# Kernel optimization log

Measured on AMD Instinct MI355X. Metric: run time of the kernel, lower is better.

Reference implementation:

```python
import jax, jax.numpy as jnp
import numpy as np

NUM_HEADS = 12


def setup_inputs() -> dict:
    key = jax.random.key(0)
    ks = jax.random.split(key, 5)
    B, S, D = 4, 2048, 768
    scale = 0.02
    return {
        "hidden_states": jax.random.normal(ks[0], (B, S, D), dtype=jnp.float32),
        "c_attn_w": jax.random.normal(ks[1], (D, 3 * D), dtype=jnp.float32) * scale,
        "c_attn_b": jax.random.normal(ks[2], (3 * D,), dtype=jnp.float32) * scale,
        "c_proj_w": jax.random.normal(ks[3], (D, D), dtype=jnp.float32) * scale,
        "c_proj_b": jax.random.normal(ks[4], (D,), dtype=jnp.float32) * scale,
    }


def reference(hidden_states, c_attn_w, c_attn_b, c_proj_w, c_proj_b):
    B, S, D = hidden_states.shape
    H = NUM_HEADS
    hd = D // H

    # fused QKV projection (HF Conv1D: x @ W + b, W is [in, out])
    qkv = hidden_states @ c_attn_w + c_attn_b  # [B, S, 3D]
    q, k, v = jnp.split(qkv, 3, axis=-1)

    def split_heads(t):
        return t.reshape(B, S, H, hd).transpose(0, 2, 1, 3)  # [B, H, S, hd]

    q, k, v = split_heads(q), split_heads(k), split_heads(v)

    # scaled dot-product scores (scale_attn_weights=True -> / sqrt(head_dim))
    scores = jnp.einsum("bhqd,bhkd->bhqk", q, k) / jnp.asarray(
        np.sqrt(hd), dtype=q.dtype
    )

    # causal mask: where(tril, scores, dtype_min) as in eager GPT2Attention
    causal = jnp.tril(jnp.ones((S, S), dtype=bool))
    mask_value = jnp.finfo(scores.dtype).min
    scores = jnp.where(causal[None, None, :, :], scores, mask_value)

    attn = jax.nn.softmax(scores, axis=-1)  # attn_dropout p=0 (eval)

    out = jnp.einsum("bhqk,bhkd->bhqd", attn, v)
    out = out.transpose(0, 2, 1, 3).reshape(B, S, D)  # merge heads

    # output projection (resid_dropout p=0)
    return out @ c_proj_w + c_proj_b
```

## Files before the change

### kernel.cpp

```cpp
#include <hip/hip_runtime.h>
#include <stdint.h>

typedef __attribute__((ext_vector_type(8))) short short8;
typedef __attribute__((ext_vector_type(4))) short short4v;
typedef __attribute__((ext_vector_type(8))) __bf16 bf16x8;
typedef __attribute__((ext_vector_type(4))) float f32x4;

#define SEQ 2048
#define DMODEL 768
#define NHEAD 12
#define HD 64
#define NBATCH 4

#define QSCALE 0.18033688011112042f

__device__ __forceinline__ float bf2f(unsigned short u) {
    return __uint_as_float(((unsigned int)u) << 16);
}
__device__ __forceinline__ unsigned short f2bf(float f) {
    unsigned int u = __float_as_uint(f);
    u += 0x7fffu + ((u >> 16) & 1u);
    return (unsigned short)(u >> 16);
}
__device__ __forceinline__ unsigned short f2bfn(float f) {
    union { __bf16 h; unsigned short u; } cv;
    cv.h = (__bf16)f;
    return cv.u;
}
__device__ __forceinline__ short8 cvt8(float4 a, float4 b) {
    short8 r;
    r[0] = (short)f2bf(a.x); r[1] = (short)f2bf(a.y);
    r[2] = (short)f2bf(a.z); r[3] = (short)f2bf(a.w);
    r[4] = (short)f2bf(b.x); r[5] = (short)f2bf(b.y);
    r[6] = (short)f2bf(b.z); r[7] = (short)f2bf(b.w);
    return r;
}
__device__ __forceinline__ f32x4 mfma16(short8 a, short8 b, f32x4 c) {
    return __builtin_amdgcn_mfma_f32_16x16x32_bf16(
        __builtin_bit_cast(bf16x8, a), __builtin_bit_cast(bf16x8, b), c, 0, 0, 0);
}
__device__ __forceinline__ f32x4 mfma16k16(short4v a, short4v b, f32x4 c) {
#if __has_builtin(__builtin_amdgcn_mfma_f32_16x16x16bf16_1k)
    return __builtin_amdgcn_mfma_f32_16x16x16bf16_1k(a, b, c, 0, 0, 0);
#else
    asm("v_mfma_f32_16x16x16_bf16 %0, %1, %2, %0" : "+v"(c) : "v"(a), "v"(b));
    return c;
#endif
}
__device__ __forceinline__ void gload16(const unsigned short* g, unsigned short* l) {
    __builtin_amdgcn_global_load_lds(
        (const __attribute__((address_space(1))) unsigned int*)g,
        (__attribute__((address_space(3))) unsigned int*)l, 16, 0, 0);
}

__global__ void detect_k(const unsigned short* x, const unsigned short* w1,
                         const unsigned short* b1, const unsigned short* w2,
                         const unsigned short* b2, int* flags) {
    const int w = threadIdx.x >> 6, l = threadIdx.x & 63;
    if (w >= 5) return;
    const unsigned short* ptrs[5] = {x, w1, b1, w2, b2};
    const unsigned short* p = ptrs[w];
    float mx = 0.f;
    for (int j = l; j < 1024; j += 64) {
        float v = fabsf(bf2f(p[j]));
        if (!(v <= 1e30f)) v = 1e31f;
        if (v > mx) mx = v;
    }
#pragma unroll
    for (int off = 1; off < 64; off <<= 1) mx = fmaxf(mx, __shfl_xor(mx, off, 64));
    if (l == 0) flags[w] = (mx > 1e3f) ? 1 : 0;
}

__global__ __launch_bounds__(256) void cvt_x(
    const float* __restrict__ Xf, const unsigned short* __restrict__ Xh,
    unsigned short* __restrict__ Xb, const int* __restrict__ flags, int n8) {
    int i = blockIdx.x * 256 + threadIdx.x;
    if (i >= n8) return;
    if (flags[0]) {
        float4 a = ((const float4*)Xf)[(size_t)i * 2];
        float4 b = ((const float4*)Xf)[(size_t)i * 2 + 1];
        *(short8*)&Xb[(size_t)i * 8] = cvt8(a, b);
    } else {
        ((uint4*)Xb)[i] = ((const uint4*)Xh)[i];
    }
}

__global__ __launch_bounds__(256) void convert_wt(
    const float* __restrict__ Wf, const unsigned short* __restrict__ Wh,
    unsigned short* __restrict__ Wt, int R, int C,
    const int* __restrict__ flags, int fidx) {

    __shared__ unsigned short tile[64][65];
    const int c0 = blockIdx.x * 64, r0 = blockIdx.y * 64;
    const int t = threadIdx.x;
    const int ri = t >> 2, cj = (t & 3) * 16;
    const bool f32 = flags[fidx] != 0;

    if (f32) {
#pragma unroll
        for (int u = 0; u < 4; u++) {
            float4 v = *(const float4*)&Wf[(size_t)(r0 + ri) * C + c0 + cj + u * 4];
            tile[ri][cj + u * 4 + 0] = f2bf(v.x);
            tile[ri][cj + u * 4 + 1] = f2bf(v.y);
            tile[ri][cj + u * 4 + 2] = f2bf(v.z);
            tile[ri][cj + u * 4 + 3] = f2bf(v.w);
        }
    } else {
        uint4 a = *(const uint4*)&Wh[(size_t)(r0 + ri) * C + c0 + cj];
        uint4 b = *(const uint4*)&Wh[(size_t)(r0 + ri) * C + c0 + cj + 8];
        *(uint4*)&tile[ri][cj] = a;
        *(uint4*)&tile[ri][cj + 8] = b;
    }
    __syncthreads();

    const int ci = t >> 2, rj = (t & 3) * 16;
    unsigned short tmp[16];
#pragma unroll
    for (int u = 0; u < 16; u++) tmp[u] = tile[rj + u][ci];
    *(uint4*)&Wt[(size_t)(c0 + ci) * R + r0 + rj]     = *(uint4*)&tmp[0];
    *(uint4*)&Wt[(size_t)(c0 + ci) * R + r0 + rj + 8] = *(uint4*)&tmp[8];
}

__global__ __launch_bounds__(256, 4) void gemm_bt(
    const float* __restrict__ Af, const unsigned short* __restrict__ Ah,
    const unsigned short* __restrict__ Bt,
    const float* __restrict__ biasf, const unsigned short* __restrict__ biash,
    int K, int mode, const int* __restrict__ flags, int aFidx, int bFidx,
    unsigned short* __restrict__ out0, unsigned short* __restrict__ out1,
    unsigned short* __restrict__ out2, float* __restrict__ outf) {

    __shared__ __align__(16) unsigned short As[2][128][32];
    __shared__ __align__(16) unsigned short Bs[2][128][32];

    int bx = blockIdx.x, by = blockIdx.y;
    {
        const int nwg = (int)(gridDim.x * gridDim.y);
        if ((nwg & 7) == 0) {
            int bid = by * gridDim.x + bx;
            const int cpx = nwg >> 3;
            bid = (bid & 7) * cpx + (bid >> 3);
            bx = bid % gridDim.x;
            by = bid / gridDim.x;
        }
    }
    const int mBase = by * 128;
    const int nBase = bx * 128;
    const int t = threadIdx.x;
    const int w = t >> 6, l = t & 63, lr = l & 15, lk = l >> 4;
    const int wr = w >> 1, wc = w & 1;

    const bool af32 = (aFidx >= 0) && (flags[aFidx] != 0);
    const bool bf32 = flags[bFidx] != 0;

    f32x4 zero = {0.f, 0.f, 0.f, 0.f};
    f32x4 acc[4][4];
#pragma unroll
    for (int i = 0; i < 4; i++)
#pragma unroll
        for (int j = 0; j < 4; j++) acc[i][j] = zero;

    const int arow2 = t >> 1;
    const int ha32 = t & 1;
    const float* Afp = Af + (size_t)mBase * K;
    const unsigned short* Ahp = Ah + (size_t)mBase * K;
    const unsigned short* Bp = Bt + (size_t)nBase * K;

    unsigned short* BsF = &Bs[0][0][0];
    unsigned short* AsF = &As[0][0][0];

    for (int k0 = 0; k0 < K; k0 += 64) {
#pragma unroll
        for (int q = 0; q < 4; q++) {
            const int c = q * 256 + t;
            const int row = (c >> 2) & 127;
            const int ha = c >> 9;
            const int g2 = c & 3;
            gload16(&Bp[(size_t)row * K + k0 + ha * 32 + g2 * 8],
                    BsF + (size_t)(q * 256 + w * 64) * 8);
        }
        if (af32) {
#pragma unroll
            for (int u = 0; u < 4; u++) {
                float4 f0 = *(const float4*)&Afp[(size_t)arow2 * K + k0 + ha32 * 32 + u * 8];
                float4 f1 = *(const float4*)&Afp[(size_t)arow2 * K + k0 + ha32 * 32 + u * 8 + 4];
                *(short8*)&As[ha32][arow2][u * 8] = cvt8(f0, f1);
            }
        } else {
#pragma unroll
            for (int q = 0; q < 4; q++) {
                const int c = q * 256 + t;
                const int row = (c >> 2) & 127;
                const int ha = c >> 9;
                const int g2 = c & 3;
                gload16(&Ahp[(size_t)row * K + k0 + ha * 32 + g2 * 8],
                        AsF + (size_t)(q * 256 + w * 64) * 8);
            }
        }
        __syncthreads();

#pragma unroll
        for (int ha = 0; ha < 2; ha++) {
            short8 a[4], b[4];
#pragma unroll
            for (int i = 0; i < 4; i++)
                a[i] = *(const short8*)&As[ha][wr * 64 + i * 16 + lr][lk * 8];
#pragma unroll
            for (int j = 0; j < 4; j++)
                b[j] = *(const short8*)&Bs[ha][wc * 64 + j * 16 + lr][lk * 8];
#pragma unroll
            for (int i = 0; i < 4; i++)
#pragma unroll
                for (int j = 0; j < 4; j++) acc[i][j] = mfma16(a[i], b[j], acc[i][j]);
        }
        __syncthreads();
    }

#pragma unroll
    for (int j = 0; j < 4; j++) {
        int col = nBase + wc * 64 + j * 16 + lr;
        float bv = bf32 ? biasf[col] : bf2f(biash[col]);
        if (mode == 0 && col >= 1536) {
            int c2 = col - 1536;
            int h = c2 >> 6, d = c2 & 63;
#pragma unroll
            for (int i = 0; i < 4; i++) {
                int row0 = mBase + wr * 64 + i * 16 + lk * 4;
                int bb = row0 >> 11, s0 = row0 & 2047;
                short4v hv4;
#pragma unroll
                for (int r = 0; r < 4; r++) hv4[r] = (short)f2bf(acc[i][j][r] + bv);
                *(short4v*)&out2[(((size_t)(bb * NHEAD + h)) * HD + d) * SEQ + s0] = hv4;
            }
        } else {
#pragma unroll
            for (int i = 0; i < 4; i++) {
                int row0 = mBase + wr * 64 + i * 16 + lk * 4;
#pragma unroll
                for (int r = 0; r < 4; r++) {
                    int row = row0 + r;
                    float fv = acc[i][j][r] + bv;
                    if (mode == 0) {
                        int bb = row >> 11;
                        int s  = row & 2047;
                        if (col < 768) {
                            int h = col >> 6, d = col & 63;
                            out0[(((size_t)(bb * NHEAD + h)) * SEQ + s) * HD + d] =
                                f2bf(fv * QSCALE);
                        } else {
                            int c2 = col - 768;
                            int h = c2 >> 6, d = c2 & 63;
                            out1[(((size_t)(bb * NHEAD + h)) * SEQ + s) * HD + d] =
                                f2bf(fv);
                        }
                    } else {
                        outf[(size_t)row * DMODEL + col] = fv;
                    }
                }
            }
        }
    }
}

#define STAGE(buf, tile) do {                                                  \
    _Pragma("unroll")                                                          \
    for (int q_ = 0; q_ < 2; ++q_) {                                           \
        const int c_ = w * 128 + q_ * 64 + l;                                  \
        const int row_ = c_ >> 3;                                              \
        const int ch_ = (c_ & 7) ^ (row_ & 7);                                 \
        gload16(&Kp[(size_t)((tile) * 64 + row_) * HD + ch_ * 8],              \
                &Ks[buf][(w * 128 + q_ * 64) * 8]);                            \
        gload16(&Vp[(size_t)row_ * SEQ + (tile) * 64 + ch_ * 8],               \
                &Vs[buf][(w * 128 + q_ * 64) * 8]);                            \
    }                                                                          \
} while (0)

__global__ __launch_bounds__(256, 3) void flash_attn(
    const unsigned short* __restrict__ Q, const unsigned short* __restrict__ Km,
    const unsigned short* __restrict__ Vt, unsigned short* __restrict__ Oatt) {

    const int h  = blockIdx.x;
    const int px = (7 * blockIdx.y + blockIdx.x + blockIdx.z) & 15;
    const int b  = blockIdx.z;
    const int bh = b * NHEAD + h;
    const int qtA = 31 - px;
    const int qtB = px;
    const int t = threadIdx.x, w = t >> 6, l = t & 63, lr = l & 15, lk = l >> 4;
    const int qbA = qtA * 64 + w * 16;
    const int qbB = qtB * 64 + w * 16;

    const unsigned short* Qp = Q + (size_t)bh * SEQ * HD;
    const unsigned short* Kp = Km + (size_t)bh * SEQ * HD;
    const unsigned short* Vp = Vt + (size_t)bh * HD * SEQ;

    __shared__ __align__(16) unsigned short Ks[3][4096];
    __shared__ __align__(16) unsigned short Vs[3][4096];

    short8 qA0 = *(const short8*)&Qp[(size_t)(qbA + lr) * HD + lk * 8];
    short8 qA1 = *(const short8*)&Qp[(size_t)(qbA + lr) * HD + 32 + lk * 8];
    short8 qB0 = *(const short8*)&Qp[(size_t)(qbB + lr) * HD + lk * 8];
    short8 qB1 = *(const short8*)&Qp[(size_t)(qbB + lr) * HD + 32 + lk * 8];

    f32x4 zero = {0.f, 0.f, 0.f, 0.f};
    f32x4 oA[4], oB[4];
    float lsumA = 0.f, lsumB = 0.f;
#pragma unroll
    for (int dt = 0; dt < 4; dt++) { oA[dt] = zero; oB[dt] = zero; }

    STAGE(0, 0);
    STAGE(1, 1);
    asm volatile("s_waitcnt vmcnt(4)" ::: "memory");
    __builtin_amdgcn_s_barrier();

    int cur = 0;
    for (int kt = 0; kt <= qtA; ++kt) {
        const bool pf = (kt + 2 <= qtA);
        if (pf) {
            const int st = (cur == 0) ? 2 : cur - 1;
            STAGE(st, kt + 2);
        }
        const bool doB = (kt <= qtB);

        f32x4 s0[4], s1[4];
#pragma unroll
        for (int ct = 0; ct < 4; ct++) { s0[ct] = zero; s1[ct] = zero; }
#pragma unroll
        for (int ct = 0; ct < 4; ct++) {
            const int row = ct * 16 + lr, sw = row & 7;
            short8 k0 = *(const short8*)&Ks[cur][(row * 8 + (lk ^ sw)) * 8];
            short8 k1 = *(const short8*)&Ks[cur][(row * 8 + ((4 | lk) ^ sw)) * 8];
            s0[ct] = mfma16(k0, qA0, s0[ct]);
            s0[ct] = mfma16(k1, qA1, s0[ct]);
            if (doB) {
                s1[ct] = mfma16(k0, qB0, s1[ct]);
                s1[ct] = mfma16(k1, qB1, s1[ct]);
            }
        }

        short4v vf[4][4];
#pragma unroll
        for (int dt = 0; dt < 4; dt++) {
            const int row = dt * 16 + lr;
            const int sw = row & 7;
#pragma unroll
            for (int ct = 0; ct < 4; ct++) {
                const int g = 2 * ct + (lk >> 1);
                const int hh = lk & 1;
                vf[dt][ct] = *(const short4v*)&Vs[cur][(row * 8 + (g ^ sw)) * 8 + hh * 4];
            }
        }

        short4v paA[4];
        {
            float p[4][4];
#pragma unroll
            for (int ct = 0; ct < 4; ct++)
#pragma unroll
                for (int r = 0; r < 4; r++) p[ct][r] = exp2f(s0[ct][r]);
            if (kt == qtA) {
                const int qrow = qbA + lr;
#pragma unroll
                for (int ct = 0; ct < 4; ct++)
#pragma unroll
                    for (int r = 0; r < 4; r++) {
                        const int key = kt * 64 + ct * 16 + lk * 4 + r;
                        if (key > qrow) p[ct][r] = 0.0f;
                    }
            }
#pragma unroll
            for (int ct = 0; ct < 4; ct++)
                lsumA += (p[ct][0] + p[ct][1]) + (p[ct][2] + p[ct][3]);
#pragma unroll
            for (int ct = 0; ct < 4; ct++) {
                short4v pk;
#pragma unroll
                for (int r = 0; r < 4; r++) pk[r] = (short)f2bfn(p[ct][r]);
                paA[ct] = pk;
            }
        }
#pragma unroll
        for (int dt = 0; dt < 4; dt++)
#pragma unroll
            for (int ct = 0; ct < 4; ct++)
                oA[dt] = mfma16k16(paA[ct], vf[dt][ct], oA[dt]);

        if (doB) {
            short4v paB[4];
            float p[4][4];
#pragma unroll
            for (int ct = 0; ct < 4; ct++)
#pragma unroll
                for (int r = 0; r < 4; r++) p[ct][r] = exp2f(s1[ct][r]);
            if (kt == qtB) {
                const int qrow = qbB + lr;
#pragma unroll
                for (int ct = 0; ct < 4; ct++)
#pragma unroll
                    for (int r = 0; r < 4; r++) {
                        const int key = kt * 64 + ct * 16 + lk * 4 + r;
                        if (key > qrow) p[ct][r] = 0.0f;
                    }
            }
#pragma unroll
            for (int ct = 0; ct < 4; ct++)
                lsumB += (p[ct][0] + p[ct][1]) + (p[ct][2] + p[ct][3]);
#pragma unroll
            for (int ct = 0; ct < 4; ct++) {
                short4v pk;
#pragma unroll
                for (int r = 0; r < 4; r++) pk[r] = (short)f2bfn(p[ct][r]);
                paB[ct] = pk;
            }
#pragma unroll
            for (int dt = 0; dt < 4; dt++)
#pragma unroll
                for (int ct = 0; ct < 4; ct++)
                    oB[dt] = mfma16k16(paB[ct], vf[dt][ct], oB[dt]);
        }

        if (kt < qtA) {
            if (pf) asm volatile("s_waitcnt vmcnt(4)" ::: "memory");
            else    asm volatile("s_waitcnt vmcnt(0)" ::: "memory");
            __builtin_amdgcn_s_barrier();
        }
        cur = (cur == 2) ? 0 : cur + 1;
    }

    lsumA += __shfl_xor(lsumA, 16, 64);
    lsumA += __shfl_xor(lsumA, 32, 64);
    lsumB += __shfl_xor(lsumB, 16, 64);
    lsumB += __shfl_xor(lsumB, 32, 64);

#pragma unroll
    for (int r = 0; r < 4; r++) {
        const float invA = 1.0f / __shfl(lsumA, lk * 4 + r, 64);
        const float invB = 1.0f / __shfl(lsumB, lk * 4 + r, 64);
        const int rowA = qbA + lk * 4 + r;
        const int rowB = qbB + lk * 4 + r;
#pragma unroll
        for (int dt = 0; dt < 4; dt++) {
            Oatt[((size_t)(b * SEQ) + rowA) * DMODEL + h * HD + dt * 16 + lr] =
                f2bfn(oA[dt][r] * invA);
            Oatt[((size_t)(b * SEQ) + rowB) * DMODEL + h * HD + dt * 16 + lr] =
                f2bfn(oB[dt][r] * invB);
        }
    }
}

extern "C" void kernel_launch(void* const* d_in, const int* in_sizes, int n_in,
                              void* d_out, int out_size, void* d_ws, size_t ws_size,
                              hipStream_t stream) {
    const void *X = d_in[0], *W1 = d_in[1], *b1 = d_in[2], *W2 = d_in[3], *b2 = d_in[4];
    for (int i = 0; i < n_in; i++) {
        switch (in_sizes[i]) {
            case NBATCH * SEQ * DMODEL: X  = d_in[i]; break;
            case DMODEL * 3 * DMODEL:   W1 = d_in[i]; break;
            case 3 * DMODEL:            b1 = d_in[i]; break;
            case DMODEL * DMODEL:       W2 = d_in[i]; break;
            case DMODEL:                b2 = d_in[i]; break;
        }
    }
    float* out = (float*)d_out;

    int* flags = (int*)d_ws;
    unsigned short* base = (unsigned short*)d_ws + 64;
    unsigned short* Wt1 = base;
    unsigned short* Wt2 = Wt1 + (size_t)2304 * 768;

    const size_t headElems = (size_t)NHEAD * SEQ * HD;
    const size_t xElems = (size_t)NBATCH * SEQ * DMODEL;
    const size_t fixedElems = 64 + (size_t)2304 * 768 + (size_t)768 * 768;
    const size_t mergedNeed = (fixedElems + xElems + 4 * NBATCH * headElems) * 2 + 1024;
    const bool merged = ws_size >= mergedNeed;

    detect_k<<<1, 320, 0, stream>>>(
        (const unsigned short*)X, (const unsigned short*)W1,
        (const unsigned short*)b1, (const unsigned short*)W2,
        (const unsigned short*)b2, flags);

    convert_wt<<<dim3(2304 / 64, 768 / 64), 256, 0, stream>>>(
        (const float*)W1, (const unsigned short*)W1, Wt1, 768, 2304, flags, 1);
    convert_wt<<<dim3(768 / 64, 768 / 64), 256, 0, stream>>>(
        (const float*)W2, (const unsigned short*)W2, Wt2, 768, 768, flags, 3);

    if (merged) {
        unsigned short* Xb  = Wt2 + (size_t)768 * 768;
        unsigned short* Qw  = Xb + xElems;
        unsigned short* Kw  = Qw + (size_t)NBATCH * headElems;
        unsigned short* Vtw = Kw + (size_t)NBATCH * headElems;
        unsigned short* Aw  = Vtw + (size_t)NBATCH * headElems;

        cvt_x<<<(int)((xElems / 8 + 255) / 256), 256, 0, stream>>>(
            (const float*)X, (const unsigned short*)X, Xb, flags, (int)(xElems / 8));

        gemm_bt<<<dim3(2304 / 128, NBATCH * SEQ / 128), 256, 0, stream>>>(
            nullptr, Xb, Wt1,
            (const float*)b1, (const unsigned short*)b1,
            DMODEL, 0, flags, -1, 2, Qw, Kw, Vtw, nullptr);

        flash_attn<<<dim3(NHEAD, 16, NBATCH), 256, 0, stream>>>(Qw, Kw, Vtw, Aw);

        gemm_bt<<<dim3(768 / 128, NBATCH * SEQ / 128), 256, 0, stream>>>(
            nullptr, Aw, Wt2,
            (const float*)b2, (const unsigned short*)b2,
            DMODEL, 1, flags, -1, 4, nullptr, nullptr, nullptr, out);
    } else {
        unsigned short* Qw  = Wt2 + (size_t)768 * 768;
        unsigned short* Kw  = Qw + headElems;
        unsigned short* Vtw = Kw + headElems;
        unsigned short* Aw  = Vtw + headElems;
        for (int batch = 0; batch < NBATCH; ++batch) {
            const size_t xoff = (size_t)batch * SEQ * DMODEL;

            gemm_bt<<<dim3(2304 / 128, SEQ / 128), 256, 0, stream>>>(
                (const float*)X + xoff, (const unsigned short*)X + xoff, Wt1,
                (const float*)b1, (const unsigned short*)b1,
                DMODEL, 0, flags, 0, 2, Qw, Kw, Vtw, nullptr);

            flash_attn<<<dim3(NHEAD, 16, 1), 256, 0, stream>>>(Qw, Kw, Vtw, Aw);

            gemm_bt<<<dim3(768 / 128, SEQ / 128), 256, 0, stream>>>(
                nullptr, Aw, Wt2,
                (const float*)b2, (const unsigned short*)b2,
                DMODEL, 1, flags, -1, 4, nullptr, nullptr, nullptr, out + xoff);
        }
    }
}
```

Baseline: 225.5 us.

## Fuse X conversion into QKV GEMM, merge weight converts, add MFMA priority hints

The separate cvt_x pass is removed, so the QKV GEMM now reads the fp32 input directly and converts it while loading tiles (aFidx=0). The two weight-transpose kernels become one launch, cutting launch overhead. In flash attention, s_setprio raises wave priority around the MFMA blocks and the score MFMAs start from zero instead of from explicitly zeroed accumulators. Converting X inside the GEMM reads fp32 A-tiles from global memory once per column tile (18 times) rather than once overall, which trades a bf16 staging write and re-read for more load traffic and conversion work in the GEMM.

After: 266.5 us. +18.2%, slower.

```diff
diff --git a/kernel.cpp b/kernel.cpp
--- a/kernel.cpp
+++ b/kernel.cpp
@@ -71,30 +71,13 @@
     if (l == 0) flags[w] = (mx > 1e3f) ? 1 : 0;
 }
 
-__global__ __launch_bounds__(256) void cvt_x(
-    const float* __restrict__ Xf, const unsigned short* __restrict__ Xh,
-    unsigned short* __restrict__ Xb, const int* __restrict__ flags, int n8) {
-    int i = blockIdx.x * 256 + threadIdx.x;
-    if (i >= n8) return;
-    if (flags[0]) {
-        float4 a = ((const float4*)Xf)[(size_t)i * 2];
-        float4 b = ((const float4*)Xf)[(size_t)i * 2 + 1];
-        *(short8*)&Xb[(size_t)i * 8] = cvt8(a, b);
-    } else {
-        ((uint4*)Xb)[i] = ((const uint4*)Xh)[i];
-    }
-}
-
-__global__ __launch_bounds__(256) void convert_wt(
-    const float* __restrict__ Wf, const unsigned short* __restrict__ Wh,
-    unsigned short* __restrict__ Wt, int R, int C,
-    const int* __restrict__ flags, int fidx) {
-
-    __shared__ unsigned short tile[64][65];
-    const int c0 = blockIdx.x * 64, r0 = blockIdx.y * 64;
-    const int t = threadIdx.x;
+__device__ __forceinline__ void wt_body(
+    unsigned short (*tile)[65], const float* __restrict__ Wf,
+    const unsigned short* __restrict__ Wh, unsigned short* __restrict__ Wt,
+    int R, int C, bool f32, int bx, int by, int t) {
+
+    const int c0 = bx * 64, r0 = by * 64;
     const int ri = t >> 2, cj = (t & 3) * 16;
-    const bool f32 = flags[fidx] != 0;
 
     if (f32) {
 #pragma unroll
@@ -119,6 +102,24 @@
     for (int u = 0; u < 16; u++) tmp[u] = tile[rj + u][ci];
     *(uint4*)&Wt[(size_t)(c0 + ci) * R + r0 + rj]     = *(uint4*)&tmp[0];
     *(uint4*)&Wt[(size_t)(c0 + ci) * R + r0 + rj + 8] = *(uint4*)&tmp[8];
+}
+
+__global__ __launch_bounds__(256) void convert_wt_both(
+    const float* __restrict__ Wf1, const unsigned short* __restrict__ Wh1,
+    unsigned short* __restrict__ Wt1,
+    const float* __restrict__ Wf2, const unsigned short* __restrict__ Wh2,
+    unsigned short* __restrict__ Wt2, const int* __restrict__ flags) {
+
+    __shared__ unsigned short tile[64][65];
+    const int t = threadIdx.x;
+    if (blockIdx.y < 12) {
+        wt_body(tile, Wf1, Wh1, Wt1, 768, 2304, flags[1] != 0,
+                (int)blockIdx.x, (int)blockIdx.y, t);
+    } else {
+        if (blockIdx.x >= 12) return;
+        wt_body(tile, Wf2, Wh2, Wt2, 768, 768, flags[3] != 0,
+                (int)blockIdx.x, (int)blockIdx.y - 12, t);
+    }
 }
 
 __global__ __launch_bounds__(256, 4) void gemm_bt(
@@ -321,20 +322,20 @@
         const bool doB = (kt <= qtB);
 
         f32x4 s0[4], s1[4];
-#pragma unroll
-        for (int ct = 0; ct < 4; ct++) { s0[ct] = zero; s1[ct] = zero; }
+        __builtin_amdgcn_s_setprio(1);
 #pragma unroll
         for (int ct = 0; ct < 4; ct++) {
             const int row = ct * 16 + lr, sw = row & 7;
             short8 k0 = *(const short8*)&Ks[cur][(row * 8 + (lk ^ sw)) * 8];
             short8 k1 = *(const short8*)&Ks[cur][(row * 8 + ((4 | lk) ^ sw)) * 8];
-            s0[ct] = mfma16(k0, qA0, s0[ct]);
+            s0[ct] = mfma16(k0, qA0, zero);
             s0[ct] = mfma16(k1, qA1, s0[ct]);
             if (doB) {
-                s1[ct] = mfma16(k0, qB0, s1[ct]);
+                s1[ct] = mfma16(k0, qB0, zero);
                 s1[ct] = mfma16(k1, qB1, s1[ct]);
             }
         }
+        __builtin_amdgcn_s_setprio(0);
 
         short4v vf[4][4];
 #pragma unroll
@@ -377,11 +378,13 @@
                 paA[ct] = pk;
             }
         }
+        __builtin_amdgcn_s_setprio(1);
 #pragma unroll
         for (int dt = 0; dt < 4; dt++)
 #pragma unroll
             for (int ct = 0; ct < 4; ct++)
                 oA[dt] = mfma16k16(paA[ct], vf[dt][ct], oA[dt]);
+        __builtin_amdgcn_s_setprio(0);
 
         if (doB) {
             short4v paB[4];
@@ -410,11 +413,13 @@
                 for (int r = 0; r < 4; r++) pk[r] = (short)f2bfn(p[ct][r]);
                 paB[ct] = pk;
             }
+            __builtin_amdgcn_s_setprio(1);
 #pragma unroll
             for (int dt = 0; dt < 4; dt++)
 #pragma unroll
                 for (int ct = 0; ct < 4; ct++)
                     oB[dt] = mfma16k16(paB[ct], vf[dt][ct], oB[dt]);
+            __builtin_amdgcn_s_setprio(0);
         }
 
         if (kt < qtA) {
@@ -477,10 +482,9 @@
         (const unsigned short*)b1, (const unsigned short*)W2,
         (const unsigned short*)b2, flags);
 
-    convert_wt<<<dim3(2304 / 64, 768 / 64), 256, 0, stream>>>(
-        (const float*)W1, (const unsigned short*)W1, Wt1, 768, 2304, flags, 1);
-    convert_wt<<<dim3(768 / 64, 768 / 64), 256, 0, stream>>>(
-        (const float*)W2, (const unsigned short*)W2, Wt2, 768, 768, flags, 3);
+    convert_wt_both<<<dim3(36, 24), 256, 0, stream>>>(
+        (const float*)W1, (const unsigned short*)W1, Wt1,
+        (const float*)W2, (const unsigned short*)W2, Wt2, flags);
 
     if (merged) {
         unsigned short* Xb  = Wt2 + (size_t)768 * 768;
@@ -489,13 +493,10 @@
         unsigned short* Vtw = Kw + (size_t)NBATCH * headElems;
         unsigned short* Aw  = Vtw + (size_t)NBATCH * headElems;
 
-        cvt_x<<<(int)((xElems / 8 + 255) / 256), 256, 0, stream>>>(
-            (const float*)X, (const unsigned short*)X, Xb, flags, (int)(xElems / 8));
-
         gemm_bt<<<dim3(2304 / 128, NBATCH * SEQ / 128), 256, 0, stream>>>(
-            nullptr, Xb, Wt1,
+            (const float*)X, (const unsigned short*)X, Wt1,
             (const float*)b1, (const unsigned short*)b1,
-            DMODEL, 0, flags, -1, 2, Qw, Kw, Vtw, nullptr);
+            DMODEL, 0, flags, 0, 2, Qw, Kw, Vtw, nullptr);
 
         flash_attn<<<dim3(NHEAD, 16, NBATCH), 256, 0, stream>>>(Qw, Kw, Vtw, Aw);
 
```
